# Kernel tuning notes

Hardware: AMD Instinct MI355X
Metric: run time of the kernel (lower is better)

Reference implementation:

```python
import jax, jax.numpy as jnp
import numpy as np

B, DIM, H, W = 8, 256, 128, 128
HEADS, D = 8, 32  # num_heads, qkv_dim (key_dim); multi_q_dim = HEADS*D = DIM


def setup_inputs() -> dict:
    key = jax.random.key(0)
    ks = jax.random.split(key, 10)
    def affine(k, n):
        k1, k2 = jax.random.split(k)
        return (1.0 + 0.1 * jax.random.normal(k1, (n,), jnp.float32),
                0.1 * jax.random.normal(k2, (n,), jnp.float32))
    q_scale, q_bias = affine(ks[1], HEADS * D)
    kv_scale, kv_bias = affine(ks[3], D)
    p_scale, p_bias = affine(ks[5], DIM)
    return {
        "input_": jax.random.normal(ks[0], (B, DIM, H, W), jnp.float32),
        "wq": jax.random.normal(ks[6], (HEADS * D, DIM), jnp.float32) / np.sqrt(DIM),
        "q_scale": q_scale, "q_bias": q_bias,
        "wkv": jax.random.normal(ks[7], (D, DIM), jnp.float32) / np.sqrt(DIM),
        "kv_scale": kv_scale, "kv_bias": kv_bias,
        "wp": jax.random.normal(ks[8], (DIM, HEADS * D), jnp.float32) / np.sqrt(HEADS * D),
        "p_scale": p_scale, "p_bias": p_bias,
    }


def conv1x1_bn(x_flat, w, scale, bias):
    # x_flat: [B,C,N]; 1x1 conv (no bias) fused with eval-mode BN affine
    y = jnp.einsum('oc,bcn->bon', w, x_flat)
    return y * scale[:, None] + bias[:, None]


def reference(input_, wq, q_scale, q_bias, wkv, kv_scale, kv_bias, wp, p_scale, p_bias):
    b, c, h, w = input_.shape
    n = h * w
    xf = input_.reshape(b, c, n)
    # queries: [B, heads, D, N]
    q = conv1x1_bn(xf, wq, q_scale, q_bias).reshape(b, HEADS, D, n)
    # shared key/value, one kv head: [B, D, N]
    kv = conv1x1_bn(xf, wkv, kv_scale, kv_bias)
    key_sm = jax.nn.softmax(kv, axis=2)      # softmax over spatial N
    query_sm = jax.nn.softmax(q, axis=2)     # softmax over channel D
    # context = softmax(K) @ V^T : [B, D, D]
    context = jnp.einsum('bdn,ben->bde', key_sm, kv)
    # attended = context^T @ Q (context broadcast over heads): [B, heads, D, N]
    attended = jnp.einsum('bde,bhdn->bhen', context, query_sm)
    av = attended.reshape(b, HEADS * D, n)
    out = conv1x1_bn(jax.nn.relu(av), wp, p_scale, p_bias)
    return out.reshape(b, c, h, w)
```

## Files before the change

kernel.cpp:

```cpp
#include <hip/hip_runtime.h>
#include <hip/hip_bf16.h>

typedef __attribute__((ext_vector_type(8))) short bf16x8;
typedef __attribute__((ext_vector_type(4))) float f32x4;

#define NB 8
#define NC 256
#define ND 32
#define NN 16384
#define TILE_P 32

#define MFMA16(a, b, c) __builtin_amdgcn_mfma_f32_16x16x32_bf16((a), (b), (c), 0, 0, 0)

__device__ __forceinline__ float u2f(unsigned short u) {
  union { unsigned int i; float f; } v; v.i = ((unsigned int)u) << 16; return v.f;
}
__device__ __forceinline__ unsigned short f2u(float f) {
  union { float f; unsigned int i; } v; v.f = f;
  unsigned int x = v.i;
  return (unsigned short)((x + 0x7fffu + ((x >> 16) & 1u)) >> 16);
}
__device__ __forceinline__ float ldg(const void* p, size_t i, int isbf) {
  return isbf ? u2f(((const unsigned short*)p)[i]) : ((const float*)p)[i];
}
__device__ __forceinline__ char* lds_at(char* base, int p, int colb) {
  return base + (p << 9) + (colb ^ ((p & 7) << 4));
}

__global__ __launch_bounds__(256) void detect_kernel(const void* __restrict__ x,
                                                     int* __restrict__ flag) {
  __shared__ int red[4];
  const unsigned int* w = (const unsigned int*)x;
  int cnt = 0;
  for (int i = threadIdx.x; i < 4096; i += 256) {
    unsigned int e = (w[i] >> 7) & 0xFFu;
    cnt += (e >= 100u && e <= 135u) ? 1 : 0;
  }
  for (int off = 32; off; off >>= 1) cnt += __shfl_xor(cnt, off, 64);
  if ((threadIdx.x & 63) == 0) red[threadIdx.x >> 6] = cnt;
  __syncthreads();
  if (threadIdx.x == 0)
    flag[0] = (red[0] + red[1] + red[2] + red[3] > 2048) ? 1 : 0;
}

__global__ __launch_bounds__(256) void prep_weights(
    const void* __restrict__ wq, const void* __restrict__ wp,
    const void* __restrict__ wkv, const int* __restrict__ flag,
    unsigned short* __restrict__ WqPh, unsigned short* __restrict__ WqPl,
    unsigned short* __restrict__ WpPh, unsigned short* __restrict__ WpPl,
    unsigned short* __restrict__ WkPh, unsigned short* __restrict__ WkPl) {
  int isbf = flag[0];
  int idx = blockIdx.x * 256 + threadIdx.x;
  const void* w;
  unsigned short *Ph, *Pl;
  int slot, o, k0;
  if (idx < 16384) {
    int mat = idx >> 13;
    slot = idx & 8191;
    int lane = slot & 63;
    int mbkt = slot >> 6;
    int mb = mbkt & 15, kt = mbkt >> 4;
    o = mb * 16 + (lane & 15);
    k0 = kt * 32 + (lane >> 4) * 8;
    w = mat ? wp : wq;
    Ph = mat ? WpPh : WqPh;
    Pl = mat ? WpPl : WqPl;
  } else {
    slot = idx - 16384;
    int lane = slot & 63;
    int grp = slot >> 6;
    int mb = grp & 1, kt = grp >> 1;
    o = mb * 16 + (lane & 15);
    k0 = kt * 32 + (lane >> 4) * 8;
    w = wkv;
    Ph = WkPh;
    Pl = WkPl;
  }
  unsigned short h[8], lo[8];
#pragma unroll
  for (int e = 0; e < 8; e++) {
    float v = ldg(w, (size_t)o * NC + k0 + e, isbf);
    unsigned short hh = f2u(v);
    h[e] = hh;
    lo[e] = isbf ? (unsigned short)0 : f2u(v - u2f(hh));
  }
  uint4 ph, pl;
  ph.x = h[0] | ((unsigned)h[1] << 16);
  ph.y = h[2] | ((unsigned)h[3] << 16);
  ph.z = h[4] | ((unsigned)h[5] << 16);
  ph.w = h[6] | ((unsigned)h[7] << 16);
  pl.x = lo[0] | ((unsigned)lo[1] << 16);
  pl.y = lo[2] | ((unsigned)lo[3] << 16);
  pl.z = lo[4] | ((unsigned)lo[5] << 16);
  pl.w = lo[6] | ((unsigned)lo[7] << 16);
  *(uint4*)(Ph + (size_t)slot * 8) = ph;
  *(uint4*)(Pl + (size_t)slot * 8) = pl;
}

template <int ISBF>
__global__ __launch_bounds__(256, 4) void kv_ctx(
    const void* __restrict__ x, const unsigned short* __restrict__ WkPh,
    const unsigned short* __restrict__ WkPl, const void* __restrict__ kv_scale,
    const void* __restrict__ kv_bias, const int* __restrict__ flag,
    float* __restrict__ Spart, float* __restrict__ Zpart) {
  __shared__ __align__(16) char pool[32768];
  if (flag[0] != ISBF) return;
  const int tid = threadIdx.x;
  const int bid = blockIdx.x;
  const int b = bid >> 7;
  const int nbase = (bid & 127) * 128;
  const int w = tid >> 6, l = tid & 63, g = l >> 4, cc = l & 15;
  const int mi = w >> 1, ni = w & 1;
  const f32x4 zero4 = {0.f, 0.f, 0.f, 0.f};
  const bf16x8* Ah = (const bf16x8*)WkPh;
  const bf16x8* Al = (const bf16x8*)WkPl;

  float scl[4], bia[4];
#pragma unroll
  for (int rr = 0; rr < 4; rr++) {
    int d = mi * 16 + 4 * g + rr;
    scl[rr] = ldg(kv_scale, d, ISBF);
    bia[rr] = ldg(kv_bias, d, ISBF);
  }

  f32x4 sacc = zero4;
  float zacc[4] = {0.f, 0.f, 0.f, 0.f};

  for (int st = 0; st < 4; st++) {
    const int n0 = nbase + st * 32;
    {
      const int c0 = (tid >> 3) * 8;
      const int pq = (tid & 7) * 4;
      unsigned short hi[8][4], lo[8][4];
      if (ISBF) {
        const unsigned short* xp =
            (const unsigned short*)x + ((size_t)(b * NC + c0)) * NN + n0 + pq;
#pragma unroll
        for (int i = 0; i < 8; i++) {
          ushort4 r = *(const ushort4*)(xp + (size_t)i * NN);
          hi[i][0] = r.x; hi[i][1] = r.y; hi[i][2] = r.z; hi[i][3] = r.w;
        }
      } else {
        const float* xp = (const float*)x + ((size_t)(b * NC + c0)) * NN + n0 + pq;
#pragma unroll
        for (int i = 0; i < 8; i++) {
          float4 v = *(const float4*)(xp + (size_t)i * NN);
          float vv[4] = {v.x, v.y, v.z, v.w};
#pragma unroll
          for (int j = 0; j < 4; j++) {
            unsigned short hh = f2u(vv[j]);
            hi[i][j] = hh;
            lo[i][j] = f2u(vv[j] - u2f(hh));
          }
        }
      }
#pragma unroll
      for (int j = 0; j < 4; j++) {
        int p = pq + j;
        uint4 wv;
        wv.x = hi[0][j] | ((unsigned)hi[1][j] << 16);
        wv.y = hi[2][j] | ((unsigned)hi[3][j] << 16);
        wv.z = hi[4][j] | ((unsigned)hi[5][j] << 16);
        wv.w = hi[6][j] | ((unsigned)hi[7][j] << 16);
        *(uint4*)lds_at(pool, p, c0 * 2) = wv;
        if (!ISBF) {
          uint4 wl2;
          wl2.x = lo[0][j] | ((unsigned)lo[1][j] << 16);
          wl2.y = lo[2][j] | ((unsigned)lo[3][j] << 16);
          wl2.z = lo[4][j] | ((unsigned)lo[5][j] << 16);
          wl2.w = lo[6][j] | ((unsigned)lo[7][j] << 16);
          *(uint4*)lds_at(pool + 16384, p, c0 * 2) = wl2;
        }
      }
    }
    __syncthreads();

    f32x4 acc = zero4;
#pragma unroll
    for (int kt = 0; kt < 8; kt++) {
      bf16x8 xb = *(const bf16x8*)lds_at(pool, ni * 16 + cc, kt * 64 + 16 * g);
      bf16x8 a = Ah[(kt * 2 + mi) * 64 + l];
      acc = MFMA16(a, xb, acc);
      if (!ISBF) {
        bf16x8 xl = *(const bf16x8*)lds_at(pool + 16384, ni * 16 + cc, kt * 64 + 16 * g);
        bf16x8 al = Al[(kt * 2 + mi) * 64 + l];
        acc = MFMA16(a, xl, acc);
        acc = MFMA16(al, xb, acc);
      }
    }

    unsigned short khv[4], klv[4], ehv[4], elv[4];
#pragma unroll
    for (int rr = 0; rr < 4; rr++) {
      float v = acc[rr] * scl[rr] + bia[rr];
      unsigned short kh = f2u(v);
      khv[rr] = kh;
      klv[rr] = f2u(v - u2f(kh));
      float e = __expf(v);
      zacc[rr] += e;
      unsigned short eh = f2u(e);
      ehv[rr] = eh;
      elv[rr] = f2u(e - u2f(eh));
    }
    __syncthreads();

    {
      char* Eh = pool;
      char* El = pool + 2048;
      char* Kh = pool + 4096;
      char* Kl = pool + 6144;
      int px = ni * 16 + cc;
#pragma unroll
      for (int rr = 0; rr < 4; rr++) {
        int d = mi * 16 + 4 * g + rr;
        int off = d * 64 + ((px * 2) ^ ((d & 3) << 4));
        *(unsigned short*)(Eh + off) = ehv[rr];
        *(unsigned short*)(El + off) = elv[rr];
        *(unsigned short*)(Kh + off) = khv[rr];
        *(unsigned short*)(Kl + off) = klv[rr];
      }
    }
    __syncthreads();

    {
      char* Eh = pool;
      char* El = pool + 2048;
      char* Kh = pool + 4096;
      char* Kl = pool + 6144;
      int ra = mi * 16 + cc;
      int rb = ni * 16 + cc;
      int ca = (16 * g) ^ ((ra & 3) << 4);
      int cb = (16 * g) ^ ((rb & 3) << 4);
      bf16x8 aEh = *(const bf16x8*)(Eh + ra * 64 + ca);
      bf16x8 aEl = *(const bf16x8*)(El + ra * 64 + ca);
      bf16x8 bKh = *(const bf16x8*)(Kh + rb * 64 + cb);
      bf16x8 bKl = *(const bf16x8*)(Kl + rb * 64 + cb);
      sacc = MFMA16(aEh, bKh, sacc);
      sacc = MFMA16(aEh, bKl, sacc);
      sacc = MFMA16(aEl, bKh, sacc);
    }
    __syncthreads();
  }

#pragma unroll
  for (int rr = 0; rr < 4; rr++) {
    zacc[rr] += __shfl_xor(zacc[rr], 1, 64);
    zacc[rr] += __shfl_xor(zacc[rr], 2, 64);
    zacc[rr] += __shfl_xor(zacc[rr], 4, 64);
    zacc[rr] += __shfl_xor(zacc[rr], 8, 64);
  }
  if (cc == 0) {
#pragma unroll
    for (int rr = 0; rr < 4; rr++)
      Zpart[((size_t)bid * 2 + ni) * ND + mi * 16 + 4 * g + rr] = zacc[rr];
  }
  {
    float* sp = Spart + (size_t)bid * 1024;
#pragma unroll
    for (int rr = 0; rr < 4; rr++)
      sp[(mi * 16 + 4 * g + rr) * 32 + ni * 16 + cc] = sacc[rr];
  }
}

__global__ __launch_bounds__(256) void ctx_redfin(const float* __restrict__ Spart,
                                                  const float* __restrict__ Zpart,
                                                  float* __restrict__ ctx) {
  __shared__ float rs[256], rz[256];
  const int bid = blockIdx.x;
  const int b = bid >> 5, d = bid & 31;
  const int t = threadIdx.x, e = t & 31, j = t >> 5;
  float s = 0.f;
  for (int c = j; c < 128; c += 8)
    s += Spart[((size_t)(b * 128 + c)) * 1024 + d * 32 + e];
  float z = Zpart[((size_t)(b * 256 + t)) * ND + d];
  rs[t] = s; rz[t] = z;
  __syncthreads();
  if (t < 128) { rs[t] += rs[t + 128]; rz[t] += rz[t + 128]; }
  __syncthreads();
  if (t < 64) { rs[t] += rs[t + 64]; rz[t] += rz[t + 64]; }
  __syncthreads();
  if (t < 32) {
    float ss = rs[t] + rs[t + 32];
    float zz = rz[t] + rz[t + 32];
    zz += __shfl_xor(zz, 1, 64);
    zz += __shfl_xor(zz, 2, 64);
    zz += __shfl_xor(zz, 4, 64);
    zz += __shfl_xor(zz, 8, 64);
    zz += __shfl_xor(zz, 16, 64);
    ctx[((size_t)b * ND + d) * ND + t] = ss / zz;
  }
}

template <int ISBF>
__global__ __launch_bounds__(256, 2) void fused_main(
    const void* __restrict__ x,
    const unsigned short* __restrict__ WqPh, const unsigned short* __restrict__ WqPl,
    const unsigned short* __restrict__ WpPh, const unsigned short* __restrict__ WpPl,
    const void* __restrict__ q_scale, const void* __restrict__ q_bias,
    const void* __restrict__ p_scale, const void* __restrict__ p_bias,
    const float* __restrict__ ctx, const int* __restrict__ flag,
    void* __restrict__ out) {
  constexpr int XT_O = 0;
  constexpr int XTL_O = 16384;
  constexpr int SMH_O = ISBF ? 16384 : 32768;
  constexpr int SML_O = ISBF ? 32768 : 49152;
  constexpr int YTH_O = 0;
  constexpr int YTL_O = 16384;
  constexpr int OT_O = ISBF ? 16384 : 32768;
  constexpr int OT_STR = ISBF ? 88 : 132;
  constexpr int POOL = ISBF ? 49152 : 69632;
  __shared__ __align__(16) char pool[POOL];
  __shared__ float qs_l[NC], qb_l[NC], ps_l[NC], pb_l[NC];
  if (flag[0] != ISBF) return;
  const int tid = threadIdx.x;
  const int b = blockIdx.x >> 9;
  const int n0 = (blockIdx.x & 511) * TILE_P;
  const int w = tid >> 6;
  const int l = tid & 63;
  const int g = l >> 4;
  const int cc = l & 15;
  const f32x4 zero4 = {0.f, 0.f, 0.f, 0.f};

  qs_l[tid] = ldg(q_scale, tid, ISBF);
  qb_l[tid] = ldg(q_bias, tid, ISBF);
  ps_l[tid] = ldg(p_scale, tid, ISBF);
  pb_l[tid] = ldg(p_bias, tid, ISBF);

  bf16x8 cAh[2], cAl[2];
  {
    const float* cb = ctx + (size_t)b * ND * ND;
#pragma unroll
    for (int mp = 0; mp < 2; mp++) {
      bf16x8 ah, al;
#pragma unroll
      for (int el = 0; el < 8; el++) {
        float v = cb[(8 * g + el) * ND + 16 * mp + cc];
        unsigned short hh = f2u(v);
        ah[el] = (short)hh;
        al[el] = (short)f2u(v - u2f(hh));
      }
      cAh[mp] = ah; cAl[mp] = al;
    }
  }

  {
    const int c0 = (tid >> 3) * 8;
    const int pq = (tid & 7) * 4;
    unsigned short hi[8][4], lo[8][4];
    if (ISBF) {
      const unsigned short* xp =
          (const unsigned short*)x + ((size_t)(b * NC + c0)) * NN + n0 + pq;
#pragma unroll
      for (int i = 0; i < 8; i++) {
        ushort4 r = *(const ushort4*)(xp + (size_t)i * NN);
        hi[i][0] = r.x; hi[i][1] = r.y; hi[i][2] = r.z; hi[i][3] = r.w;
      }
    } else {
      const float* xp = (const float*)x + ((size_t)(b * NC + c0)) * NN + n0 + pq;
#pragma unroll
      for (int i = 0; i < 8; i++) {
        float4 v = *(const float4*)(xp + (size_t)i * NN);
        float vv[4] = {v.x, v.y, v.z, v.w};
#pragma unroll
        for (int j = 0; j < 4; j++) {
          unsigned short hh = f2u(vv[j]);
          hi[i][j] = hh;
          lo[i][j] = f2u(vv[j] - u2f(hh));
        }
      }
    }
#pragma unroll
    for (int j = 0; j < 4; j++) {
      int p = pq + j;
      uint4 wv;
      wv.x = hi[0][j] | ((unsigned)hi[1][j] << 16);
      wv.y = hi[2][j] | ((unsigned)hi[3][j] << 16);
      wv.z = hi[4][j] | ((unsigned)hi[5][j] << 16);
      wv.w = hi[6][j] | ((unsigned)hi[7][j] << 16);
      *(uint4*)lds_at(pool + XT_O, p, c0 * 2) = wv;
      if (!ISBF) {
        uint4 wl2;
        wl2.x = lo[0][j] | ((unsigned)lo[1][j] << 16);
        wl2.y = lo[2][j] | ((unsigned)lo[3][j] << 16);
        wl2.z = lo[4][j] | ((unsigned)lo[5][j] << 16);
        wl2.w = lo[6][j] | ((unsigned)lo[7][j] << 16);
        *(uint4*)lds_at(pool + XTL_O, p, c0 * 2) = wl2;
      }
    }
  }
  __syncthreads();

  f32x4 acc[4][2];
#pragma unroll
  for (int mi = 0; mi < 4; mi++) { acc[mi][0] = zero4; acc[mi][1] = zero4; }
  {
    const bf16x8* Aq = (const bf16x8*)WqPh;
    const bf16x8* Aql = (const bf16x8*)WqPl;
#pragma unroll
    for (int kt = 0; kt < 8; kt++) {
      bf16x8 xb0 = *(const bf16x8*)lds_at(pool + XT_O, cc, kt * 64 + 16 * g);
      bf16x8 xb1 = *(const bf16x8*)lds_at(pool + XT_O, 16 + cc, kt * 64 + 16 * g);
      bf16x8 av[4];
#pragma unroll
      for (int mi = 0; mi < 4; mi++) av[mi] = Aq[(kt * 16 + w * 4 + mi) * 64 + l];
#pragma unroll
      for (int mi = 0; mi < 4; mi++) {
        acc[mi][0] = MFMA16(av[mi], xb0, acc[mi][0]);
        acc[mi][1] = MFMA16(av[mi], xb1, acc[mi][1]);
      }
      if (!ISBF) {
        bf16x8 xl0 = *(const bf16x8*)lds_at(pool + XTL_O, cc, kt * 64 + 16 * g);
        bf16x8 xl1 = *(const bf16x8*)lds_at(pool + XTL_O, 16 + cc, kt * 64 + 16 * g);
#pragma unroll
        for (int mi = 0; mi < 4; mi++) {
          bf16x8 al2 = Aql[(kt * 16 + w * 4 + mi) * 64 + l];
          acc[mi][0] = MFMA16(av[mi], xl0, acc[mi][0]);
          acc[mi][1] = MFMA16(av[mi], xl1, acc[mi][1]);
          acc[mi][0] = MFMA16(al2, xb0, acc[mi][0]);
          acc[mi][1] = MFMA16(al2, xb1, acc[mi][1]);
        }
      }
    }
  }

  float inv_s[2][2];
#pragma unroll
  for (int hp = 0; hp < 2; hp++) {
#pragma unroll
    for (int ni = 0; ni < 2; ni++) {
      float e8[8];
      float mx = -3.0e38f;
#pragma unroll
      for (int mi2 = 0; mi2 < 2; mi2++) {
#pragma unroll
        for (int r = 0; r < 4; r++) {
          int o = w * 64 + (2 * hp + mi2) * 16 + 4 * g + r;
          float v = acc[2 * hp + mi2][ni][r] * qs_l[o] + qb_l[o];
          e8[mi2 * 4 + r] = v;
          mx = fmaxf(mx, v);
        }
      }
      mx = fmaxf(mx, __shfl_xor(mx, 16, 64));
      mx = fmaxf(mx, __shfl_xor(mx, 32, 64));
      float s = 0.f;
#pragma unroll
      for (int i2 = 0; i2 < 8; i2++) { e8[i2] = __expf(e8[i2] - mx); s += e8[i2]; }
      s += __shfl_xor(s, 16, 64);
      s += __shfl_xor(s, 32, 64);
      inv_s[hp][ni] = 1.f / s;
      int p = ni * 16 + cc;
#pragma unroll
      for (int mi2 = 0; mi2 < 2; mi2++) {
        int colb = (w * 64 + (2 * hp + mi2) * 16 + 4 * g) * 2;
        unsigned short h[4], lo2[4];
#pragma unroll
        for (int r = 0; r < 4; r++) {
          float ev = e8[mi2 * 4 + r];
          unsigned short hh = f2u(ev);
          h[r] = hh;
          lo2[r] = f2u(ev - u2f(hh));
        }
        uint2 wh, wl2;
        wh.x = h[0] | ((unsigned)h[1] << 16);
        wh.y = h[2] | ((unsigned)h[3] << 16);
        wl2.x = lo2[0] | ((unsigned)lo2[1] << 16);
        wl2.y = lo2[2] | ((unsigned)lo2[3] << 16);
        *(uint2*)lds_at(pool + SMH_O, p, colb) = wh;
        *(uint2*)lds_at(pool + SML_O, p, colb) = wl2;
      }
    }
  }
  __syncthreads();

#pragma unroll
  for (int hp = 0; hp < 2; hp++) {
    f32x4 cacc[2][2];
#pragma unroll
    for (int mp = 0; mp < 2; mp++) { cacc[mp][0] = zero4; cacc[mp][1] = zero4; }
#pragma unroll
    for (int ni = 0; ni < 2; ni++) {
      int p = ni * 16 + cc;
      int colb = ((2 * w + hp) * 32 + 8 * g) * 2;
      bf16x8 bh = *(const bf16x8*)lds_at(pool + SMH_O, p, colb);
      bf16x8 bl = *(const bf16x8*)lds_at(pool + SML_O, p, colb);
#pragma unroll
      for (int mp = 0; mp < 2; mp++) {
        cacc[mp][ni] = MFMA16(cAh[mp], bh, cacc[mp][ni]);
        cacc[mp][ni] = MFMA16(cAh[mp], bl, cacc[mp][ni]);
        cacc[mp][ni] = MFMA16(cAl[mp], bh, cacc[mp][ni]);
      }
    }
#pragma unroll
    for (int mp = 0; mp < 2; mp++) {
#pragma unroll
      for (int ni = 0; ni < 2; ni++) {
        int p = ni * 16 + cc;
        float iv = inv_s[hp][ni];
        unsigned short h[4], lo2[4];
#pragma unroll
        for (int r = 0; r < 4; r++) {
          float y = fmaxf(cacc[mp][ni][r] * iv, 0.f);
          unsigned short hh = f2u(y);
          h[r] = hh;
          lo2[r] = f2u(y - u2f(hh));
        }
        int colb = ((2 * w + hp) * 32 + mp * 16 + 4 * g) * 2;
        uint2 wh;
        wh.x = h[0] | ((unsigned)h[1] << 16);
        wh.y = h[2] | ((unsigned)h[3] << 16);
        *(uint2*)lds_at(pool + YTH_O, p, colb) = wh;
        uint2 wl2;
        wl2.x = lo2[0] | ((unsigned)lo2[1] << 16);
        wl2.y = lo2[2] | ((unsigned)lo2[3] << 16);
        *(uint2*)lds_at(pool + YTL_O, p, colb) = wl2;
      }
    }
  }
  __syncthreads();

  f32x4 oacc[4][2];
#pragma unroll
  for (int mi = 0; mi < 4; mi++) { oacc[mi][0] = zero4; oacc[mi][1] = zero4; }
  {
    const bf16x8* Ap = (const bf16x8*)WpPh;
    const bf16x8* Apl = (const bf16x8*)WpPl;
#pragma unroll
    for (int kt = 0; kt < 8; kt++) {
      bf16x8 yh0 = *(const bf16x8*)lds_at(pool + YTH_O, cc, kt * 64 + 16 * g);
      bf16x8 yh1 = *(const bf16x8*)lds_at(pool + YTH_O, 16 + cc, kt * 64 + 16 * g);
      bf16x8 yl0 = *(const bf16x8*)lds_at(pool + YTL_O, cc, kt * 64 + 16 * g);
      bf16x8 yl1 = *(const bf16x8*)lds_at(pool + YTL_O, 16 + cc, kt * 64 + 16 * g);
      bf16x8 av[4];
#pragma unroll
      for (int mi = 0; mi < 4; mi++) av[mi] = Ap[(kt * 16 + w * 4 + mi) * 64 + l];
#pragma unroll
      for (int mi = 0; mi < 4; mi++) {
        oacc[mi][0] = MFMA16(av[mi], yh0, oacc[mi][0]);
        oacc[mi][1] = MFMA16(av[mi], yh1, oacc[mi][1]);
        oacc[mi][0] = MFMA16(av[mi], yl0, oacc[mi][0]);
        oacc[mi][1] = MFMA16(av[mi], yl1, oacc[mi][1]);
      }
      if (!ISBF) {
#pragma unroll
        for (int mi = 0; mi < 4; mi++) {
          bf16x8 al2 = Apl[(kt * 16 + w * 4 + mi) * 64 + l];
          oacc[mi][0] = MFMA16(al2, yh0, oacc[mi][0]);
          oacc[mi][1] = MFMA16(al2, yh1, oacc[mi][1]);
        }
      }
    }
  }

  {
    char* OT = pool + OT_O;
#pragma unroll
    for (int mi = 0; mi < 4; mi++) {
#pragma unroll
      for (int ni = 0; ni < 2; ni++) {
#pragma unroll
        for (int r = 0; r < 4; r++) {
          int o = w * 64 + mi * 16 + 4 * g + r;
          float v = oacc[mi][ni][r] * ps_l[o] + pb_l[o];
          int p = ni * 16 + cc;
          if (ISBF)
            *(unsigned short*)(OT + o * OT_STR + p * 2) = f2u(v);
          else
            *(float*)(OT + o * OT_STR + p * 4) = v;
        }
      }
    }
  }
  __syncthreads();
  {
    char* OT = pool + OT_O;
    int o = tid;
    size_t gbase = ((size_t)(b * NC + o)) * NN + n0;
    if (ISBF) {
      unsigned short* po = (unsigned short*)out + gbase;
#pragma unroll
      for (int k = 0; k < 4; k++) {
        uint2 a = *(const uint2*)(OT + o * OT_STR + k * 16);
        uint2 b2 = *(const uint2*)(OT + o * OT_STR + k * 16 + 8);
        *(uint4*)(po + k * 8) = make_uint4(a.x, a.y, b2.x, b2.y);
      }
    } else {
      float* po = (float*)out + gbase;
#pragma unroll
      for (int k = 0; k < 8; k++) {
        float4 v;
        v.x = *(const float*)(OT + o * OT_STR + (k * 4 + 0) * 4);
        v.y = *(const float*)(OT + o * OT_STR + (k * 4 + 1) * 4);
        v.z = *(const float*)(OT + o * OT_STR + (k * 4 + 2) * 4);
        v.w = *(const float*)(OT + o * OT_STR + (k * 4 + 3) * 4);
        *(float4*)(po + k * 4) = v;
      }
    }
  }
}

extern "C" void kernel_launch(void* const* d_in, const int* in_sizes, int n_in,
                              void* d_out, int out_size, void* d_ws, size_t ws_size,
                              hipStream_t stream) {
  const void* input   = d_in[0];
  const void* wq      = d_in[1];
  const void* q_scale = d_in[2];
  const void* q_bias  = d_in[3];
  const void* wkv     = d_in[4];
  const void* kv_scale= d_in[5];
  const void* kv_bias = d_in[6];
  const void* wp      = d_in[7];
  const void* p_scale = d_in[8];
  const void* p_bias  = d_in[9];

  char* w = (char*)d_ws;
  int*  flag = (int*)w;      w += 256;
  float* Spart = (float*)w;  w += (size_t)1024 * 1024 * 4;
  float* Zpart = (float*)w;  w += (size_t)2048 * ND * 4;
  float* ctx  = (float*)w;   w += (size_t)NB * ND * ND * 4;
  unsigned short* WqPh = (unsigned short*)w; w += (size_t)NC * NC * 2;
  unsigned short* WqPl = (unsigned short*)w; w += (size_t)NC * NC * 2;
  unsigned short* WpPh = (unsigned short*)w; w += (size_t)NC * NC * 2;
  unsigned short* WpPl = (unsigned short*)w; w += (size_t)NC * NC * 2;
  unsigned short* WkPh = (unsigned short*)w; w += (size_t)ND * NC * 2;
  unsigned short* WkPl = (unsigned short*)w; w += (size_t)ND * NC * 2;

  detect_kernel<<<1, 256, 0, stream>>>(input, flag);
  prep_weights<<<68, 256, 0, stream>>>(wq, wp, wkv, flag, WqPh, WqPl, WpPh, WpPl,
                                       WkPh, WkPl);
  kv_ctx<1><<<1024, 256, 0, stream>>>(input, WkPh, WkPl, kv_scale, kv_bias, flag,
                                      Spart, Zpart);
  kv_ctx<0><<<1024, 256, 0, stream>>>(input, WkPh, WkPl, kv_scale, kv_bias, flag,
                                      Spart, Zpart);
  ctx_redfin<<<256, 256, 0, stream>>>(Spart, Zpart, ctx);
  fused_main<1><<<4096, 256, 0, stream>>>(input, WqPh, WqPl, WpPh, WpPl,
                                          q_scale, q_bias, p_scale, p_bias,
                                          ctx, flag, (void*)d_out);
  fused_main<0><<<4096, 256, 0, stream>>>(input, WqPh, WqPl, WpPh, WpPl,
                                          q_scale, q_bias, p_scale, p_bias,
                                          ctx, flag, (void*)d_out);
}
```

Baseline: 460.3 us.

## Load kv operands directly from global, trim bf16 lo-path, vectorize fp32 output

The kv_ctx kernel drops its LDS staging of the input tile. Each lane now gathers its MFMA operand straight from global memory with strided scalar loads, which removes a barrier and shrinks LDS from 32KB to 8KB, raising occupancy. In fused_main the low-part MFMAs and stores for the relu output are skipped on the bf16 path, and an extra lo×lo correction term is added on the fp32 path. The fp32 output stride is padded to 144 so each row can be read back from LDS as float4. The scalar strided global gathers may coalesce poorly compared with the old vector loads.

```diff
diff --git a/kernel.cpp b/kernel.cpp
--- a/kernel.cpp
+++ b/kernel.cpp
@@ -103,7 +103,7 @@
     const unsigned short* __restrict__ WkPl, const void* __restrict__ kv_scale,
     const void* __restrict__ kv_bias, const int* __restrict__ flag,
     float* __restrict__ Spart, float* __restrict__ Zpart) {
-  __shared__ __align__(16) char pool[32768];
+  __shared__ __align__(16) char pool[8192];
   if (flag[0] != ISBF) return;
   const int tid = threadIdx.x;
   const int bid = blockIdx.x;
@@ -126,66 +126,43 @@
   f32x4 sacc = zero4;
   float zacc[4] = {0.f, 0.f, 0.f, 0.f};
 
+  char* Eh = pool;
+  char* El = pool + 2048;
+  char* Kh = pool + 4096;
+  char* Kl = pool + 6144;
+
   for (int st = 0; st < 4; st++) {
-    const int n0 = nbase + st * 32;
-    {
-      const int c0 = (tid >> 3) * 8;
-      const int pq = (tid & 7) * 4;
-      unsigned short hi[8][4], lo[8][4];
-      if (ISBF) {
-        const unsigned short* xp =
-            (const unsigned short*)x + ((size_t)(b * NC + c0)) * NN + n0 + pq;
-#pragma unroll
-        for (int i = 0; i < 8; i++) {
-          ushort4 r = *(const ushort4*)(xp + (size_t)i * NN);
-          hi[i][0] = r.x; hi[i][1] = r.y; hi[i][2] = r.z; hi[i][3] = r.w;
-        }
-      } else {
-        const float* xp = (const float*)x + ((size_t)(b * NC + c0)) * NN + n0 + pq;
-#pragma unroll
-        for (int i = 0; i < 8; i++) {
-          float4 v = *(const float4*)(xp + (size_t)i * NN);
-          float vv[4] = {v.x, v.y, v.z, v.w};
-#pragma unroll
-          for (int j = 0; j < 4; j++) {
-            unsigned short hh = f2u(vv[j]);
-            hi[i][j] = hh;
-            lo[i][j] = f2u(vv[j] - u2f(hh));
-          }
-        }
-      }
-#pragma unroll
-      for (int j = 0; j < 4; j++) {
-        int p = pq + j;
-        uint4 wv;
-        wv.x = hi[0][j] | ((unsigned)hi[1][j] << 16);
-        wv.y = hi[2][j] | ((unsigned)hi[3][j] << 16);
-        wv.z = hi[4][j] | ((unsigned)hi[5][j] << 16);
-        wv.w = hi[6][j] | ((unsigned)hi[7][j] << 16);
-        *(uint4*)lds_at(pool, p, c0 * 2) = wv;
-        if (!ISBF) {
-          uint4 wl2;
-          wl2.x = lo[0][j] | ((unsigned)lo[1][j] << 16);
-          wl2.y = lo[2][j] | ((unsigned)lo[3][j] << 16);
-          wl2.z = lo[4][j] | ((unsigned)lo[5][j] << 16);
-          wl2.w = lo[6][j] | ((unsigned)lo[7][j] << 16);
-          *(uint4*)lds_at(pool + 16384, p, c0 * 2) = wl2;
-        }
-      }
-    }
-    __syncthreads();
+    const int px = nbase + st * 32 + ni * 16 + cc;
 
     f32x4 acc = zero4;
-#pragma unroll
-    for (int kt = 0; kt < 8; kt++) {
-      bf16x8 xb = *(const bf16x8*)lds_at(pool, ni * 16 + cc, kt * 64 + 16 * g);
-      bf16x8 a = Ah[(kt * 2 + mi) * 64 + l];
-      acc = MFMA16(a, xb, acc);
-      if (!ISBF) {
-        bf16x8 xl = *(const bf16x8*)lds_at(pool + 16384, ni * 16 + cc, kt * 64 + 16 * g);
+    if (ISBF) {
+      const unsigned short* xb =
+          (const unsigned short*)x + (size_t)b * NC * NN + px;
+#pragma unroll
+      for (int kt = 0; kt < 8; kt++) {
+        bf16x8 xh;
+#pragma unroll
+        for (int e = 0; e < 8; e++)
+          xh[e] = (short)xb[(size_t)(kt * 32 + 8 * g + e) * NN];
+        acc = MFMA16(Ah[(kt * 2 + mi) * 64 + l], xh, acc);
+      }
+    } else {
+      const float* xb = (const float*)x + (size_t)b * NC * NN + px;
+#pragma unroll
+      for (int kt = 0; kt < 8; kt++) {
+        bf16x8 xh, xl;
+#pragma unroll
+        for (int e = 0; e < 8; e++) {
+          float v = xb[(size_t)(kt * 32 + 8 * g + e) * NN];
+          unsigned short hh = f2u(v);
+          xh[e] = (short)hh;
+          xl[e] = (short)f2u(v - u2f(hh));
+        }
+        bf16x8 a = Ah[(kt * 2 + mi) * 64 + l];
         bf16x8 al = Al[(kt * 2 + mi) * 64 + l];
+        acc = MFMA16(a, xh, acc);
         acc = MFMA16(a, xl, acc);
-        acc = MFMA16(al, xb, acc);
+        acc = MFMA16(al, xh, acc);
       }
     }
 
@@ -202,18 +179,13 @@
       ehv[rr] = eh;
       elv[rr] = f2u(e - u2f(eh));
     }
-    __syncthreads();
 
     {
-      char* Eh = pool;
-      char* El = pool + 2048;
-      char* Kh = pool + 4096;
-      char* Kl = pool + 6144;
-      int px = ni * 16 + cc;
+      int pxl = ni * 16 + cc;
 #pragma unroll
       for (int rr = 0; rr < 4; rr++) {
         int d = mi * 16 + 4 * g + rr;
-        int off = d * 64 + ((px * 2) ^ ((d & 3) << 4));
+        int off = d * 64 + ((pxl * 2) ^ ((d & 3) << 4));
         *(unsigned short*)(Eh + off) = ehv[rr];
         *(unsigned short*)(El + off) = elv[rr];
         *(unsigned short*)(Kh + off) = khv[rr];
@@ -223,10 +195,6 @@
     __syncthreads();
 
     {
-      char* Eh = pool;
-      char* El = pool + 2048;
-      char* Kh = pool + 4096;
-      char* Kl = pool + 6144;
       int ra = mi * 16 + cc;
       int rb = ni * 16 + cc;
       int ca = (16 * g) ^ ((ra & 3) << 4);
@@ -307,7 +275,7 @@
   constexpr int YTH_O = 0;
   constexpr int YTL_O = 16384;
   constexpr int OT_O = ISBF ? 16384 : 32768;
-  constexpr int OT_STR = ISBF ? 88 : 132;
+  constexpr int OT_STR = ISBF ? 88 : 144;
   constexpr int POOL = ISBF ? 49152 : 69632;
   __shared__ __align__(16) char pool[POOL];
   __shared__ float qs_l[NC], qb_l[NC], ps_l[NC], pb_l[NC];
@@ -488,6 +456,7 @@
         cacc[mp][ni] = MFMA16(cAh[mp], bh, cacc[mp][ni]);
         cacc[mp][ni] = MFMA16(cAh[mp], bl, cacc[mp][ni]);
         cacc[mp][ni] = MFMA16(cAl[mp], bh, cacc[mp][ni]);
+        if (!ISBF) cacc[mp][ni] = MFMA16(cAl[mp], bl, cacc[mp][ni]);
       }
     }
 #pragma unroll
@@ -509,10 +478,12 @@
         wh.x = h[0] | ((unsigned)h[1] << 16);
         wh.y = h[2] | ((unsigned)h[3] << 16);
         *(uint2*)lds_at(pool + YTH_O, p, colb) = wh;
-        uint2 wl2;
-        wl2.x = lo2[0] | ((unsigned)lo2[1] << 16);
-        wl2.y = lo2[2] | ((unsigned)lo2[3] << 16);
-        *(uint2*)lds_at(pool + YTL_O, p, colb) = wl2;
+        if (!ISBF) {
+          uint2 wl2;
+          wl2.x = lo2[0] | ((unsigned)lo2[1] << 16);
+          wl2.y = lo2[2] | ((unsigned)lo2[3] << 16);
+          *(uint2*)lds_at(pool + YTL_O, p, colb) = wl2;
+        }
       }
     }
   }
@@ -528,8 +499,6 @@
     for (int kt = 0; kt < 8; kt++) {
       bf16x8 yh0 = *(const bf16x8*)lds_at(pool + YTH_O, cc, kt * 64 + 16 * g);
       bf16x8 yh1 = *(const bf16x8*)lds_at(pool + YTH_O, 16 + cc, kt * 64 + 16 * g);
-      bf16x8 yl0 = *(const bf16x8*)lds_at(pool + YTL_O, cc, kt * 64 + 16 * g);
-      bf16x8 yl1 = *(const bf16x8*)lds_at(pool + YTL_O, 16 + cc, kt * 64 + 16 * g);
       bf16x8 av[4];
 #pragma unroll
       for (int mi = 0; mi < 4; mi++) av[mi] = Ap[(kt * 16 + w * 4 + mi) * 64 + l];
@@ -537,13 +506,15 @@
       for (int mi = 0; mi < 4; mi++) {
         oacc[mi][0] = MFMA16(av[mi], yh0, oacc[mi][0]);
         oacc[mi][1] = MFMA16(av[mi], yh1, oacc[mi][1]);
-        oacc[mi][0] = MFMA16(av[mi], yl0, oacc[mi][0]);
-        oacc[mi][1] = MFMA16(av[mi], yl1, oacc[mi][1]);
       }
       if (!ISBF) {
+        bf16x8 yl0 = *(const bf16x8*)lds_at(pool + YTL_O, cc, kt * 64 + 16 * g);
+        bf16x8 yl1 = *(const bf16x8*)lds_at(pool + YTL_O, 16 + cc, kt * 64 + 16 * g);
 #pragma unroll
         for (int mi = 0; mi < 4; mi++) {
           bf16x8 al2 = Apl[(kt * 16 + w * 4 + mi) * 64 + l];
+          oacc[mi][0] = MFMA16(av[mi], yl0, oacc[mi][0]);
+          oacc[mi][1] = MFMA16(av[mi], yl1, oacc[mi][1]);
           oacc[mi][0] = MFMA16(al2, yh0, oacc[mi][0]);
           oacc[mi][1] = MFMA16(al2, yh1, oacc[mi][1]);
         }
@@ -586,14 +557,8 @@
     } else {
       float* po = (float*)out + gbase;
 #pragma unroll
-      for (int k = 0; k < 8; k++) {
-        float4 v;
-        v.x = *(const float*)(OT + o * OT_STR + (k * 4 + 0) * 4);
-        v.y = *(const float*)(OT + o * OT_STR + (k * 4 + 1) * 4);
-        v.z = *(const float*)(OT + o * OT_STR + (k * 4 + 2) * 4);
-        v.w = *(const float*)(OT + o * OT_STR + (k * 4 + 3) * 4);
-        *(float4*)(po + k * 4) = v;
-      }
+      for (int k = 0; k < 8; k++)
+        *(float4*)(po + k * 4) = *(const float4*)(OT + o * OT_STR + k * 16);
     }
   }
 }
```

Measured after the change: 447.8 us. 2.7% less time.
